# Optimization experiments

Hardware: AMD Instinct MI355X
Metric: run time of the kernel (lower is better)

Reference implementation:

```python
import jax, jax.numpy as jnp
import numpy as np

NUM_EXPERTS = 8
HIDDEN = 1024
INTER = 2048
RANK = 8
LORA_ALPHA = 16
SCALING = LORA_ALPHA / RANK  # 2.0


def setup_inputs() -> dict:
    key = jax.random.key(0)
    ks = jax.random.split(key, 7)
    return {
        "hidden_states": jax.random.normal(ks[0], (NUM_EXPERTS * 1024, HIDDEN), jnp.float32),
        "gate_up_proj": jax.random.normal(ks[1], (NUM_EXPERTS, HIDDEN, 2 * INTER), jnp.float32) * 0.02,
        "down_proj": jax.random.normal(ks[2], (NUM_EXPERTS, INTER, HIDDEN), jnp.float32) * 0.02,
        "lora_A_gu": jax.random.normal(ks[3], (RANK, HIDDEN), jnp.float32) * 0.02,
        "lora_B_gu": jax.random.normal(ks[4], (2 * INTER, RANK), jnp.float32) * 0.02,
        "lora_A_dn": jax.random.normal(ks[5], (RANK, INTER), jnp.float32) * 0.02,
        "lora_B_dn": jax.random.normal(ks[6], (1024, RANK), jnp.float32) * 0.02,
    }


def reference(hidden_states, gate_up_proj, down_proj, lora_A_gu, lora_B_gu, lora_A_dn, lora_B_dn):
    E, H, F2 = gate_up_proj.shape
    x = hidden_states.reshape(E, -1, H)  # [E, T, H]
    # per-expert GEMM + shared LoRA adapter (dropout inactive at eval)
    gate_up = jnp.einsum('eth,ehf->etf', x, gate_up_proj)
    gate_up = gate_up + ((x @ lora_A_gu.T) @ lora_B_gu.T) * SCALING  # [E, T, 2I]
    gate, up = jnp.split(gate_up, 2, axis=-1)
    hidden = up * jax.nn.silu(gate)  # SwiGLU, [E, T, I]
    out = jnp.einsum('eti,eih->eth', hidden, down_proj)
    out = out + ((hidden @ lora_A_dn.T) @ lora_B_dn.T) * SCALING
    return out.reshape(-1, H)
```

## Files before the change

kernel.cpp:

```cpp
#include <hip/hip_runtime.h>
#include <math.h>


#define NE 8
#define TT 1024
#define HH 1024
#define II 2048
#define FF2 4096
#define RR 8
#define NROW (NE * TT)
#define SCAL 2.0f

typedef __bf16 bf16x8 __attribute__((ext_vector_type(8)));
typedef float f32x4 __attribute__((ext_vector_type(4)));

#define GLOAD16(g, l)                                                        \
  __builtin_amdgcn_global_load_lds((const __attribute__((address_space(1))) void*)(g), \
                                   (__attribute__((address_space(3))) void*)(l), 16, 0, 0)
#define BARRIER __builtin_amdgcn_s_barrier()
#define SB0 __builtin_amdgcn_sched_barrier(0)
#define WAITV2 asm volatile("s_waitcnt vmcnt(2)" ::: "memory")
#define WAITV0 asm volatile("s_waitcnt vmcnt(0)" ::: "memory")
#define WAITL0 asm volatile("s_waitcnt lgkmcnt(0)" ::: "memory")

__device__ __forceinline__ unsigned short f2bf(float f) {
  unsigned int u = __float_as_uint(f);
  u += 0x7fffu + ((u >> 16) & 1u);
  return (unsigned short)(u >> 16);
}
__device__ __forceinline__ float dot4(float4 a, float4 b) {
  return a.x * b.x + a.y * b.y + a.z * b.z + a.w * b.w;
}

__global__ __launch_bounds__(256) void convx_kernel(const float* __restrict__ x,
                                                    unsigned short* __restrict__ xb) {
  const int i = blockIdx.x * 256 + threadIdx.x;
  const float4 a = *(const float4*)(x + (size_t)i * 8);
  const float4 b = *(const float4*)(x + (size_t)i * 8 + 4);
  union { unsigned short u[8]; uint4 v; } pk;
  pk.u[0] = f2bf(a.x); pk.u[1] = f2bf(a.y); pk.u[2] = f2bf(a.z); pk.u[3] = f2bf(a.w);
  pk.u[4] = f2bf(b.x); pk.u[5] = f2bf(b.y); pk.u[6] = f2bf(b.z); pk.u[7] = f2bf(b.w);
  *(uint4*)(xb + (size_t)i * 8) = pk.v;
}

__global__ __launch_bounds__(256) void transconv_gu_kernel(const float* __restrict__ W,
                                                           unsigned short* __restrict__ WT) {
  __shared__ float ts[64][65];
  const int bid = blockIdx.x;
  const int nt = bid & 63, kt = (bid >> 6) & 15, e = bid >> 10;
  const float* Win = W + (size_t)e * HH * FF2 + (size_t)(kt * 64) * FF2 + nt * 64;
  const int tid = threadIdx.x;
#pragma unroll
  for (int l = 0; l < 4; ++l) {
    const int idx = tid + l * 256, r = idx >> 4, c4 = idx & 15;
    const float4 v = *(const float4*)(Win + (size_t)r * FF2 + c4 * 4);
    ts[r][c4 * 4 + 0] = v.x; ts[r][c4 * 4 + 1] = v.y;
    ts[r][c4 * 4 + 2] = v.z; ts[r][c4 * 4 + 3] = v.w;
  }
  __syncthreads();
  unsigned short* We = WT + (size_t)e * FF2 * HH;
#pragma unroll
  for (int l = 0; l < 2; ++l) {
    const int idx = tid + l * 256, j = idx >> 3, q = idx & 7;
    int orow;
    if (nt < 32) orow = (nt * 4 + (j >> 4)) * 32 + (j & 15);
    else         orow = ((nt - 32) * 4 + (j >> 4)) * 32 + 16 + (j & 15);
    union { unsigned short u[8]; uint4 v; } pk;
#pragma unroll
    for (int kk = 0; kk < 8; ++kk) pk.u[kk] = f2bf(ts[q * 8 + kk][j]);
    *(uint4*)(We + (size_t)orow * HH + kt * 64 + q * 8) = pk.v;
  }
}

__global__ __launch_bounds__(256) void transconv_dn_kernel(const float* __restrict__ W,
                                                           unsigned short* __restrict__ WT) {
  __shared__ float ts[64][65];
  const int bid = blockIdx.x;
  const int nt = bid & 15, kt = (bid >> 4) & 31, e = bid >> 9;
  const float* Win = W + (size_t)e * II * HH + (size_t)(kt * 64) * HH + nt * 64;
  const int tid = threadIdx.x;
#pragma unroll
  for (int l = 0; l < 4; ++l) {
    const int idx = tid + l * 256, r = idx >> 4, c4 = idx & 15;
    const float4 v = *(const float4*)(Win + (size_t)r * HH + c4 * 4);
    ts[r][c4 * 4 + 0] = v.x; ts[r][c4 * 4 + 1] = v.y;
    ts[r][c4 * 4 + 2] = v.z; ts[r][c4 * 4 + 3] = v.w;
  }
  __syncthreads();
  unsigned short* Wout = WT + (size_t)e * HH * II + (size_t)(nt * 64) * II + kt * 64;
#pragma unroll
  for (int l = 0; l < 2; ++l) {
    const int idx = tid + l * 256, j = idx >> 3, q = idx & 7;
    union { unsigned short u[8]; uint4 v; } pk;
#pragma unroll
    for (int kk = 0; kk < 8; ++kk) pk.u[kk] = f2bf(ts[q * 8 + kk][j]);
    *(uint4*)(Wout + (size_t)j * II + q * 8) = pk.v;
  }
}

template <int K>
__global__ __launch_bounds__(256) void rowdot_kernel(const float* __restrict__ x,
                                                     const float* __restrict__ A,
                                                     float* __restrict__ xa) {
  const int w = threadIdx.x >> 6, lane = threadIdx.x & 63;
  const int t = blockIdx.x * 4 + w;
  const float* xrow = x + (size_t)t * K;
  float acc[RR];
#pragma unroll
  for (int r = 0; r < RR; ++r) acc[r] = 0.f;
#pragma unroll
  for (int c = 0; c < K / 256; ++c) {
    const float4 xv = *(const float4*)(xrow + c * 256 + lane * 4);
#pragma unroll
    for (int r = 0; r < RR; ++r) {
      const float4 av = *(const float4*)(A + (size_t)r * K + c * 256 + lane * 4);
      acc[r] += dot4(xv, av);
    }
  }
#pragma unroll
  for (int r = 0; r < RR; ++r) {
    float v = acc[r];
#pragma unroll
    for (int off = 32; off > 0; off >>= 1) v += __shfl_down(v, off, 64);
    if (lane == 0) xa[(size_t)t * RR + r] = v;
  }
}

__global__ __launch_bounds__(256) void rowdot_bf16_kernel(const unsigned short* __restrict__ h,
                                                          const float* __restrict__ A,
                                                          float* __restrict__ ha) {
  const int w = threadIdx.x >> 6, lane = threadIdx.x & 63;
  const int t = blockIdx.x * 4 + w;
  const unsigned short* hrow = h + (size_t)t * II;
  float acc[RR];
#pragma unroll
  for (int r = 0; r < RR; ++r) acc[r] = 0.f;
#pragma unroll
  for (int c = 0; c < II / 512; ++c) {
    const uint4 v = *(const uint4*)(hrow + c * 512 + lane * 8);
    float xv[8];
    xv[0] = __uint_as_float(v.x << 16); xv[1] = __uint_as_float(v.x & 0xffff0000u);
    xv[2] = __uint_as_float(v.y << 16); xv[3] = __uint_as_float(v.y & 0xffff0000u);
    xv[4] = __uint_as_float(v.z << 16); xv[5] = __uint_as_float(v.z & 0xffff0000u);
    xv[6] = __uint_as_float(v.w << 16); xv[7] = __uint_as_float(v.w & 0xffff0000u);
#pragma unroll
    for (int r = 0; r < RR; ++r) {
      const float4 a0 = *(const float4*)(A + (size_t)r * II + c * 512 + lane * 8);
      const float4 a1 = *(const float4*)(A + (size_t)r * II + c * 512 + lane * 8 + 4);
      acc[r] += xv[0] * a0.x + xv[1] * a0.y + xv[2] * a0.z + xv[3] * a0.w +
                xv[4] * a1.x + xv[5] * a1.y + xv[6] * a1.z + xv[7] * a1.w;
    }
  }
#pragma unroll
  for (int r = 0; r < RR; ++r) {
    float v = acc[r];
#pragma unroll
    for (int off = 32; off > 0; off >>= 1) v += __shfl_down(v, off, 64);
    if (lane == 0) ha[(size_t)t * RR + r] = v;
  }
}

__global__ __launch_bounds__(256) void gemm1_8p_kernel(
    const unsigned short* __restrict__ xb, const unsigned short* __restrict__ WguT,
    const float* __restrict__ xa, const float* __restrict__ Bgu,
    unsigned short* __restrict__ hidden) {
  __shared__ unsigned short sm[2][16384];

  const int bid = blockIdx.x;
  const int e = bid & 7;
  const int s = bid >> 3;
  const int g = s >> 6, wq = s & 63;
  const int tt = wq >> 3, it = (g << 3) | (wq & 7);
  const int t0 = e * TT + tt * 128;
  const unsigned short* Ag = xb + (size_t)t0 * HH;
  const unsigned short* Bg = WguT + (size_t)e * FF2 * HH + (size_t)(it * 128) * HH;

  const int tid = threadIdx.x;
  const int w = tid >> 6, lane = tid & 63;
  const int wr = w >> 1, wc = w & 1;
  const int lrow = lane & 15, lkg = lane >> 4;

  auto stageA = [&](int buf, int kt, int h) {
#pragma unroll
    for (int l = 0; l < 2; ++l) {
      const int i = tid + l * 256;
      const int r = i >> 3, sl = i & 7;
      const int row = h * 64 + r;
      GLOAD16((const char*)(Ag + (size_t)row * HH + kt * 64 + ((sl ^ (row & 7)) << 3)),
              (char*)&sm[buf][0] + row * 128 + sl * 16);
    }
  };
  auto stageB = [&](int buf, int kt, int h) {
#pragma unroll
    for (int l = 0; l < 2; ++l) {
      const int i = tid + l * 256;
      const int r = i >> 3, sl = i & 7;
      const int row = h * 64 + r;
      GLOAD16((const char*)(Bg + (size_t)row * HH + kt * 64 + ((sl ^ (row & 7)) << 3)),
              (char*)&sm[buf][0] + 16384 + row * 128 + sl * 16);
    }
  };
  auto ldA = [&](int p, int mIdx, int s2) -> bf16x8 {
    const int row = wr * 64 + mIdx * 16 + lrow;
    const int sl = (s2 * 4 + lkg) ^ (row & 7);
    return *(const bf16x8*)((const char*)&sm[p][0] + row * 128 + sl * 16);
  };
  auto ldB = [&](int p, int nj, int s2) -> bf16x8 {
    const int row = wc * 64 + nj * 16 + lrow;
    const int sl = (s2 * 4 + lkg) ^ (row & 7);
    return *(const bf16x8*)((const char*)&sm[p][0] + 16384 + row * 128 + sl * 16);
  };

  f32x4 acc[4][4];
#pragma unroll
  for (int i = 0; i < 4; ++i)
#pragma unroll
    for (int j = 0; j < 4; ++j) acc[i][j] = (f32x4)(0.f);

  stageA(0, 0, 0); stageA(0, 0, 1); stageB(0, 0, 0); stageB(0, 0, 1);

  bf16x8 af[2][2], bfr[2][2];
  const int NT = HH / 64;
  for (int t = 0; t < NT; ++t) {
    const int p = t & 1, q = p ^ 1;
    const bool pf = (t + 1 < NT);
    if (pf) { stageA(q, t + 1, 0); WAITV2; } else { WAITV0; }
    SB0; BARRIER;
#pragma unroll
    for (int mi = 0; mi < 2; ++mi) { af[mi][0] = ldA(p, mi, 0); af[mi][1] = ldA(p, mi, 1); }
#pragma unroll
    for (int nj = 0; nj < 2; ++nj) { bfr[nj][0] = ldB(p, nj, 0); bfr[nj][1] = ldB(p, nj, 1); }
    BARRIER; WAITL0; SB0;
    __builtin_amdgcn_s_setprio(1);
#pragma unroll
    for (int mi = 0; mi < 2; ++mi)
#pragma unroll
      for (int nj = 0; nj < 2; ++nj)
#pragma unroll
        for (int s2 = 0; s2 < 2; ++s2)
          acc[mi][nj] = __builtin_amdgcn_mfma_f32_16x16x32_bf16(af[mi][s2], bfr[nj][s2], acc[mi][nj], 0, 0, 0);
    __builtin_amdgcn_s_setprio(0); SB0; BARRIER;
    if (pf) stageA(q, t + 1, 1);
#pragma unroll
    for (int nj = 0; nj < 2; ++nj) { bfr[nj][0] = ldB(p, 2 + nj, 0); bfr[nj][1] = ldB(p, 2 + nj, 1); }
    BARRIER; WAITL0; SB0;
    __builtin_amdgcn_s_setprio(1);
#pragma unroll
    for (int mi = 0; mi < 2; ++mi)
#pragma unroll
      for (int nj = 0; nj < 2; ++nj)
#pragma unroll
        for (int s2 = 0; s2 < 2; ++s2)
          acc[mi][2 + nj] = __builtin_amdgcn_mfma_f32_16x16x32_bf16(af[mi][s2], bfr[nj][s2], acc[mi][2 + nj], 0, 0, 0);
    __builtin_amdgcn_s_setprio(0); SB0; BARRIER;
    if (pf) stageB(q, t + 1, 0);
#pragma unroll
    for (int mi = 0; mi < 2; ++mi) { af[mi][0] = ldA(p, 2 + mi, 0); af[mi][1] = ldA(p, 2 + mi, 1); }
    BARRIER; WAITL0; SB0;
    __builtin_amdgcn_s_setprio(1);
#pragma unroll
    for (int mi = 0; mi < 2; ++mi)
#pragma unroll
      for (int nj = 0; nj < 2; ++nj)
#pragma unroll
        for (int s2 = 0; s2 < 2; ++s2)
          acc[2 + mi][2 + nj] = __builtin_amdgcn_mfma_f32_16x16x32_bf16(af[mi][s2], bfr[nj][s2], acc[2 + mi][2 + nj], 0, 0, 0);
    __builtin_amdgcn_s_setprio(0); SB0; BARRIER;
    if (pf) stageB(q, t + 1, 1);
#pragma unroll
    for (int nj = 0; nj < 2; ++nj) { bfr[nj][0] = ldB(p, nj, 0); bfr[nj][1] = ldB(p, nj, 1); }
    BARRIER; WAITL0; SB0;
    __builtin_amdgcn_s_setprio(1);
#pragma unroll
    for (int mi = 0; mi < 2; ++mi)
#pragma unroll
      for (int nj = 0; nj < 2; ++nj)
#pragma unroll
        for (int s2 = 0; s2 < 2; ++s2)
          acc[2 + mi][nj] = __builtin_amdgcn_mfma_f32_16x16x32_bf16(af[mi][s2], bfr[nj][s2], acc[2 + mi][nj], 0, 0, 0);
    __builtin_amdgcn_s_setprio(0); SB0; BARRIER;
  }

  const float4* xa4 = (const float4*)xa;
  const float4* B4 = (const float4*)Bgu;
#pragma unroll
  for (int f = 0; f < 2; ++f) {
    const int gc = it * 64 + (wc * 2 + f) * 16 + lrow;
    const float4 bg0 = B4[gc * 2], bg1 = B4[gc * 2 + 1];
    const float4 bu0 = B4[(II + gc) * 2], bu1 = B4[(II + gc) * 2 + 1];
#pragma unroll
    for (int m = 0; m < 4; ++m) {
      const int tb = t0 + wr * 64 + m * 16 + lkg * 4;
#pragma unroll
      for (int j = 0; j < 4; ++j) {
        const int trow = tb + j;
        const float4 xr0 = xa4[trow * 2], xr1 = xa4[trow * 2 + 1];
        const float gv = acc[m][f * 2 + 0][j] + SCAL * (dot4(xr0, bg0) + dot4(xr1, bg1));
        const float uv = acc[m][f * 2 + 1][j] + SCAL * (dot4(xr0, bu0) + dot4(xr1, bu1));
        const float sg = gv / (1.f + __expf(-gv));
        hidden[(size_t)trow * II + gc] = f2bf(uv * sg);
      }
    }
  }
}

__global__ __launch_bounds__(256) void gemm2_8p_kernel(
    const unsigned short* __restrict__ hid, const unsigned short* __restrict__ WdnT,
    const float* __restrict__ ha, const float* __restrict__ Bdn,
    float* __restrict__ out) {
  __shared__ unsigned short sm[2][16384];

  const int bid = blockIdx.x;
  const int e = bid & 7;
  const int s = bid >> 3;
  const int g = s >> 4, wq = s & 15;
  const int tt = (g >> 1) * 4 + (wq >> 2);
  const int ht = (g & 1) * 4 + (wq & 3);
  const int t0 = e * TT + tt * 128;
  const int h0 = ht * 128;
  const unsigned short* Ag = hid + (size_t)t0 * II;
  const unsigned short* Bg = WdnT + (size_t)e * HH * II + (size_t)h0 * II;

  const int tid = threadIdx.x;
  const int w = tid >> 6, lane = tid & 63;
  const int wr = w >> 1, wc = w & 1;
  const int lrow = lane & 15, lkg = lane >> 4;

  auto stageA = [&](int buf, int kt, int h) {
#pragma unroll
    for (int l = 0; l < 2; ++l) {
      const int i = tid + l * 256;
      const int r = i >> 3, sl = i & 7;
      const int row = h * 64 + r;
      GLOAD16((const char*)(Ag + (size_t)row * II + kt * 64 + ((sl ^ (row & 7)) << 3)),
              (char*)&sm[buf][0] + row * 128 + sl * 16);
    }
  };
  auto stageB = [&](int buf, int kt, int h) {
#pragma unroll
    for (int l = 0; l < 2; ++l) {
      const int i = tid + l * 256;
      const int r = i >> 3, sl = i & 7;
      const int row = h * 64 + r;
      GLOAD16((const char*)(Bg + (size_t)row * II + kt * 64 + ((sl ^ (row & 7)) << 3)),
              (char*)&sm[buf][0] + 16384 + row * 128 + sl * 16);
    }
  };
  auto ldA = [&](int p, int mIdx, int s2) -> bf16x8 {
    const int row = wr * 64 + mIdx * 16 + lrow;
    const int sl = (s2 * 4 + lkg) ^ (row & 7);
    return *(const bf16x8*)((const char*)&sm[p][0] + row * 128 + sl * 16);
  };
  auto ldB = [&](int p, int nj, int s2) -> bf16x8 {
    const int row = wc * 64 + nj * 16 + lrow;
    const int sl = (s2 * 4 + lkg) ^ (row & 7);
    return *(const bf16x8*)((const char*)&sm[p][0] + 16384 + row * 128 + sl * 16);
  };

  f32x4 acc[4][4];
#pragma unroll
  for (int i = 0; i < 4; ++i)
#pragma unroll
    for (int j = 0; j < 4; ++j) acc[i][j] = (f32x4)(0.f);

  stageA(0, 0, 0); stageA(0, 0, 1); stageB(0, 0, 0); stageB(0, 0, 1);

  bf16x8 af[2][2], bfr[2][2];
  const int NT = II / 64;
  for (int t = 0; t < NT; ++t) {
    const int p = t & 1, q = p ^ 1;
    const bool pf = (t + 1 < NT);
    if (pf) { stageA(q, t + 1, 0); WAITV2; } else { WAITV0; }
    SB0; BARRIER;
#pragma unroll
    for (int mi = 0; mi < 2; ++mi) { af[mi][0] = ldA(p, mi, 0); af[mi][1] = ldA(p, mi, 1); }
#pragma unroll
    for (int nj = 0; nj < 2; ++nj) { bfr[nj][0] = ldB(p, nj, 0); bfr[nj][1] = ldB(p, nj, 1); }
    BARRIER; WAITL0; SB0;
    __builtin_amdgcn_s_setprio(1);
#pragma unroll
    for (int mi = 0; mi < 2; ++mi)
#pragma unroll
      for (int nj = 0; nj < 2; ++nj)
#pragma unroll
        for (int s2 = 0; s2 < 2; ++s2)
          acc[mi][nj] = __builtin_amdgcn_mfma_f32_16x16x32_bf16(af[mi][s2], bfr[nj][s2], acc[mi][nj], 0, 0, 0);
    __builtin_amdgcn_s_setprio(0); SB0; BARRIER;
    if (pf) stageA(q, t + 1, 1);
#pragma unroll
    for (int nj = 0; nj < 2; ++nj) { bfr[nj][0] = ldB(p, 2 + nj, 0); bfr[nj][1] = ldB(p, 2 + nj, 1); }
    BARRIER; WAITL0; SB0;
    __builtin_amdgcn_s_setprio(1);
#pragma unroll
    for (int mi = 0; mi < 2; ++mi)
#pragma unroll
      for (int nj = 0; nj < 2; ++nj)
#pragma unroll
        for (int s2 = 0; s2 < 2; ++s2)
          acc[mi][2 + nj] = __builtin_amdgcn_mfma_f32_16x16x32_bf16(af[mi][s2], bfr[nj][s2], acc[mi][2 + nj], 0, 0, 0);
    __builtin_amdgcn_s_setprio(0); SB0; BARRIER;
    if (pf) stageB(q, t + 1, 0);
#pragma unroll
    for (int mi = 0; mi < 2; ++mi) { af[mi][0] = ldA(p, 2 + mi, 0); af[mi][1] = ldA(p, 2 + mi, 1); }
    BARRIER; WAITL0; SB0;
    __builtin_amdgcn_s_setprio(1);
#pragma unroll
    for (int mi = 0; mi < 2; ++mi)
#pragma unroll
      for (int nj = 0; nj < 2; ++nj)
#pragma unroll
        for (int s2 = 0; s2 < 2; ++s2)
          acc[2 + mi][2 + nj] = __builtin_amdgcn_mfma_f32_16x16x32_bf16(af[mi][s2], bfr[nj][s2], acc[2 + mi][2 + nj], 0, 0, 0);
    __builtin_amdgcn_s_setprio(0); SB0; BARRIER;
    if (pf) stageB(q, t + 1, 1);
#pragma unroll
    for (int nj = 0; nj < 2; ++nj) { bfr[nj][0] = ldB(p, nj, 0); bfr[nj][1] = ldB(p, nj, 1); }
    BARRIER; WAITL0; SB0;
    __builtin_amdgcn_s_setprio(1);
#pragma unroll
    for (int mi = 0; mi < 2; ++mi)
#pragma unroll
      for (int nj = 0; nj < 2; ++nj)
#pragma unroll
        for (int s2 = 0; s2 < 2; ++s2)
          acc[2 + mi][nj] = __builtin_amdgcn_mfma_f32_16x16x32_bf16(af[mi][s2], bfr[nj][s2], acc[2 + mi][nj], 0, 0, 0);
    __builtin_amdgcn_s_setprio(0); SB0; BARRIER;
  }

  const float4* ha4 = (const float4*)ha;
  const float4* B4 = (const float4*)Bdn;
#pragma unroll
  for (int nj = 0; nj < 4; ++nj) {
    const int col = h0 + wc * 64 + nj * 16 + lrow;
    const float4 b0 = B4[col * 2], b1 = B4[col * 2 + 1];
#pragma unroll
    for (int m = 0; m < 4; ++m) {
      const int tb = t0 + wr * 64 + m * 16 + lkg * 4;
#pragma unroll
      for (int j = 0; j < 4; ++j) {
        const int trow = tb + j;
        const float4 hr0 = ha4[trow * 2], hr1 = ha4[trow * 2 + 1];
        out[(size_t)trow * HH + col] = acc[m][nj][j] + SCAL * (dot4(hr0, b0) + dot4(hr1, b1));
      }
    }
  }
}

__global__ __launch_bounds__(256) void gemm1_conv_kernel(const float* __restrict__ x,
                                                         const float* __restrict__ Wgu,
                                                         const float* __restrict__ xa,
                                                         const float* __restrict__ Bgu,
                                                         unsigned short* __restrict__ hidden) {
  __shared__ unsigned short As[128][40];
  __shared__ unsigned short Bs[128][40];
  const int bid = blockIdx.x;
  const int e = bid >> 8, rem = bid & 255, tt = rem >> 5, it = rem & 31;
  const int t0 = e * TT + tt * 128, i0 = it * 64;
  const float* Wg = Wgu + (size_t)e * HH * FF2;
  const int tid = threadIdx.x, w = tid >> 6, lane = tid & 63;
  const int wr = w >> 1, wc = w & 1, lrow = lane & 15, lk = (lane >> 4) * 8;
  f32x4 acc[4][4];
#pragma unroll
  for (int i = 0; i < 4; ++i)
#pragma unroll
    for (int j = 0; j < 4; ++j) acc[i][j] = (f32x4)(0.f);
  for (int k0 = 0; k0 < HH; k0 += 32) {
#pragma unroll
    for (int l = 0; l < 4; ++l) {
      const int idx = tid + l * 256, row = idx >> 3, kq = idx & 7;
      const float4 v = *(const float4*)(x + (size_t)(t0 + row) * HH + k0 + kq * 4);
      ushort4 p; p.x = f2bf(v.x); p.y = f2bf(v.y); p.z = f2bf(v.z); p.w = f2bf(v.w);
      *(ushort4*)&As[row][kq * 4] = p;
    }
#pragma unroll
    for (int l = 0; l < 2; ++l) {
      const int idx = tid + l * 256, col = idx & 127, kq8 = idx >> 7;
      const int gcol = i0 + (col & 63) + ((col >> 6) * II);
      union { unsigned short u[8]; uint4 v; } pk;
#pragma unroll
      for (int kk = 0; kk < 8; ++kk) pk.u[kk] = f2bf(Wg[(size_t)(k0 + kq8 * 8 + kk) * FF2 + gcol]);
      *(uint4*)&Bs[col][kq8 * 8] = pk.v;
    }
    __syncthreads();
    bf16x8 af[4], bfr[4];
#pragma unroll
    for (int mi = 0; mi < 4; ++mi) af[mi] = *(const bf16x8*)&As[wr * 64 + mi * 16 + lrow][lk];
#pragma unroll
    for (int nj = 0; nj < 4; ++nj) {
      const int c = (nj < 2) ? (wc * 32 + nj * 16) : (64 + wc * 32 + (nj - 2) * 16);
      bfr[nj] = *(const bf16x8*)&Bs[c + lrow][lk];
    }
#pragma unroll
    for (int mi = 0; mi < 4; ++mi)
#pragma unroll
      for (int nj = 0; nj < 4; ++nj)
        acc[mi][nj] = __builtin_amdgcn_mfma_f32_16x16x32_bf16(af[mi], bfr[nj], acc[mi][nj], 0, 0, 0);
    __syncthreads();
  }
  const float4* xa4 = (const float4*)xa;
  const float4* B4 = (const float4*)Bgu;
#pragma unroll
  for (int nj = 0; nj < 2; ++nj) {
    const int coln = i0 + wc * 32 + nj * 16 + lrow;
    const float4 bg0 = B4[coln * 2], bg1 = B4[coln * 2 + 1];
    const float4 bu0 = B4[(II + coln) * 2], bu1 = B4[(II + coln) * 2 + 1];
#pragma unroll
    for (int mi = 0; mi < 4; ++mi) {
      const int tb = t0 + wr * 64 + mi * 16 + (lane >> 4) * 4;
#pragma unroll
      for (int j = 0; j < 4; ++j) {
        const int t = tb + j;
        const float4 xr0 = xa4[t * 2], xr1 = xa4[t * 2 + 1];
        const float g = acc[mi][nj][j] + SCAL * (dot4(xr0, bg0) + dot4(xr1, bg1));
        const float u = acc[mi][nj + 2][j] + SCAL * (dot4(xr0, bu0) + dot4(xr1, bu1));
        const float s = g / (1.f + __expf(-g));
        hidden[(size_t)t * II + coln] = f2bf(u * s);
      }
    }
  }
}

__global__ __launch_bounds__(256) void gemm2_conv_kernel(const unsigned short* __restrict__ hid,
                                                         const float* __restrict__ Wdn,
                                                         const float* __restrict__ ha,
                                                         const float* __restrict__ Bdn,
                                                         float* __restrict__ out) {
  __shared__ unsigned short As[128][40];
  __shared__ unsigned short Bs[128][40];
  const int bid = blockIdx.x;
  const int e = bid >> 6, rem = bid & 63, tt = rem >> 3, ht = rem & 7;
  const int t0 = e * TT + tt * 128, h0 = ht * 128;
  const float* Wd = Wdn + (size_t)e * II * HH;
  const int tid = threadIdx.x, w = tid >> 6, lane = tid & 63;
  const int wr = w >> 1, wc = w & 1, lrow = lane & 15, lk = (lane >> 4) * 8;
  f32x4 acc[4][4];
#pragma unroll
  for (int i = 0; i < 4; ++i)
#pragma unroll
    for (int j = 0; j < 4; ++j) acc[i][j] = (f32x4)(0.f);
  for (int k0 = 0; k0 < II; k0 += 32) {
#pragma unroll
    for (int l = 0; l < 2; ++l) {
      const int idx = tid + l * 256, row = idx >> 2, kq8 = idx & 3;
      *(uint4*)&As[row][kq8 * 8] = *(const uint4*)(hid + (size_t)(t0 + row) * II + k0 + kq8 * 8);
    }
#pragma unroll
    for (int l = 0; l < 2; ++l) {
      const int idx = tid + l * 256, col = idx & 127, kq8 = idx >> 7;
      union { unsigned short u[8]; uint4 v; } pk;
#pragma unroll
      for (int kk = 0; kk < 8; ++kk) pk.u[kk] = f2bf(Wd[(size_t)(k0 + kq8 * 8 + kk) * HH + h0 + col]);
      *(uint4*)&Bs[col][kq8 * 8] = pk.v;
    }
    __syncthreads();
    bf16x8 af[4], bfr[4];
#pragma unroll
    for (int mi = 0; mi < 4; ++mi) af[mi] = *(const bf16x8*)&As[wr * 64 + mi * 16 + lrow][lk];
#pragma unroll
    for (int nj = 0; nj < 4; ++nj) bfr[nj] = *(const bf16x8*)&Bs[wc * 64 + nj * 16 + lrow][lk];
#pragma unroll
    for (int mi = 0; mi < 4; ++mi)
#pragma unroll
      for (int nj = 0; nj < 4; ++nj)
        acc[mi][nj] = __builtin_amdgcn_mfma_f32_16x16x32_bf16(af[mi], bfr[nj], acc[mi][nj], 0, 0, 0);
    __syncthreads();
  }
  const float4* ha4 = (const float4*)ha;
  const float4* B4 = (const float4*)Bdn;
#pragma unroll
  for (int nj = 0; nj < 4; ++nj) {
    const int coln = h0 + wc * 64 + nj * 16 + lrow;
    const float4 b0 = B4[coln * 2], b1 = B4[coln * 2 + 1];
#pragma unroll
    for (int mi = 0; mi < 4; ++mi) {
      const int tb = t0 + wr * 64 + mi * 16 + (lane >> 4) * 4;
#pragma unroll
      for (int j = 0; j < 4; ++j) {
        const int t = tb + j;
        const float4 hr0 = ha4[t * 2], hr1 = ha4[t * 2 + 1];
        out[(size_t)t * HH + coln] = acc[mi][nj][j] + SCAL * (dot4(hr0, b0) + dot4(hr1, b1));
      }
    }
  }
}

extern "C" void kernel_launch(void* const* d_in, const int* in_sizes, int n_in,
                              void* d_out, int out_size, void* d_ws, size_t ws_size,
                              hipStream_t stream) {
  const float* x   = (const float*)d_in[0];
  const float* Wgu = (const float*)d_in[1];
  const float* Wdn = (const float*)d_in[2];
  const float* Agu = (const float*)d_in[3];
  const float* Bgu = (const float*)d_in[4];
  const float* Adn = (const float*)d_in[5];
  const float* Bdn = (const float*)d_in[6];
  float* out = (float*)d_out;

  char* ws = (char*)d_ws;
  unsigned short* hidden = (unsigned short*)ws;
  const size_t OFF_XB  = (size_t)NROW * II * 2;
  const size_t OFF_WGU = OFF_XB + (size_t)NROW * HH * 2;
  const size_t OFF_WDN = OFF_WGU + (size_t)NE * FF2 * HH * 2;
  const size_t OFF_XA  = OFF_WDN + (size_t)NE * HH * II * 2;
  const size_t OFF_HA  = OFF_XA + (size_t)NROW * RR * 4;
  const size_t NEED    = OFF_HA + (size_t)NROW * RR * 4;

  if (ws_size >= NEED) {
    unsigned short* xb   = (unsigned short*)(ws + OFF_XB);
    unsigned short* WguT = (unsigned short*)(ws + OFF_WGU);
    unsigned short* WdnT = (unsigned short*)(ws + OFF_WDN);
    float* xa = (float*)(ws + OFF_XA);
    float* ha = (float*)(ws + OFF_HA);

    convx_kernel<<<(NROW * HH) / (256 * 8), 256, 0, stream>>>(x, xb);
    transconv_gu_kernel<<<NE * 16 * 64, 256, 0, stream>>>(Wgu, WguT);
    transconv_dn_kernel<<<NE * 32 * 16, 256, 0, stream>>>(Wdn, WdnT);
    rowdot_kernel<HH><<<NROW / 4, 256, 0, stream>>>(x, Agu, xa);
    gemm1_8p_kernel<<<NE * 8 * 32, 256, 0, stream>>>(xb, WguT, xa, Bgu, hidden);
    rowdot_bf16_kernel<<<NROW / 4, 256, 0, stream>>>(hidden, Adn, ha);
    gemm2_8p_kernel<<<NE * 8 * 8, 256, 0, stream>>>(hidden, WdnT, ha, Bdn, out);
  } else {
    float* xa = (float*)(ws + OFF_XB);
    float* ha = xa + (size_t)NROW * RR;
    rowdot_kernel<HH><<<NROW / 4, 256, 0, stream>>>(x, Agu, xa);
    gemm1_conv_kernel<<<NE * 8 * 32, 256, 0, stream>>>(x, Wgu, xa, Bgu, hidden);
    rowdot_bf16_kernel<<<NROW / 4, 256, 0, stream>>>(hidden, Adn, ha);
    gemm2_conv_kernel<<<NE * 8 * 8, 256, 0, stream>>>(hidden, Wdn, ha, Bdn, out);
  }
}
```

Before: 395.6 us.

## Collapse four-phase interleaved GEMM main loop into single prefetch-then-compute stage

```diff
diff --git a/kernel.cpp b/kernel.cpp
--- a/kernel.cpp
+++ b/kernel.cpp
@@ -19,7 +19,7 @@
                                    (__attribute__((address_space(3))) void*)(l), 16, 0, 0)
 #define BARRIER __builtin_amdgcn_s_barrier()
 #define SB0 __builtin_amdgcn_sched_barrier(0)
-#define WAITV2 asm volatile("s_waitcnt vmcnt(2)" ::: "memory")
+#define WAITV8 asm volatile("s_waitcnt vmcnt(8)" ::: "memory")
 #define WAITV0 asm volatile("s_waitcnt vmcnt(0)" ::: "memory")
 #define WAITL0 asm volatile("s_waitcnt lgkmcnt(0)" ::: "memory")
 
@@ -219,65 +219,31 @@
 
   stageA(0, 0, 0); stageA(0, 0, 1); stageB(0, 0, 0); stageB(0, 0, 1);
 
-  bf16x8 af[2][2], bfr[2][2];
   const int NT = HH / 64;
   for (int t = 0; t < NT; ++t) {
     const int p = t & 1, q = p ^ 1;
-    const bool pf = (t + 1 < NT);
-    if (pf) { stageA(q, t + 1, 0); WAITV2; } else { WAITV0; }
+    if (t + 1 < NT) {
+      stageA(q, t + 1, 0); stageA(q, t + 1, 1);
+      stageB(q, t + 1, 0); stageB(q, t + 1, 1);
+      WAITV8;
+    } else {
+      WAITV0;
+    }
     SB0; BARRIER;
-#pragma unroll
-    for (int mi = 0; mi < 2; ++mi) { af[mi][0] = ldA(p, mi, 0); af[mi][1] = ldA(p, mi, 1); }
-#pragma unroll
-    for (int nj = 0; nj < 2; ++nj) { bfr[nj][0] = ldB(p, nj, 0); bfr[nj][1] = ldB(p, nj, 1); }
-    BARRIER; WAITL0; SB0;
+    bf16x8 af[4][2], bfr[4][2];
+#pragma unroll
+    for (int mi = 0; mi < 4; ++mi) { af[mi][0] = ldA(p, mi, 0); af[mi][1] = ldA(p, mi, 1); }
+#pragma unroll
+    for (int nj = 0; nj < 4; ++nj) { bfr[nj][0] = ldB(p, nj, 0); bfr[nj][1] = ldB(p, nj, 1); }
+    WAITL0; SB0;
     __builtin_amdgcn_s_setprio(1);
 #pragma unroll
-    for (int mi = 0; mi < 2; ++mi)
-#pragma unroll
-      for (int nj = 0; nj < 2; ++nj)
+    for (int mi = 0; mi < 4; ++mi)
+#pragma unroll
+      for (int nj = 0; nj < 4; ++nj)
 #pragma unroll
         for (int s2 = 0; s2 < 2; ++s2)
           acc[mi][nj] = __builtin_amdgcn_mfma_f32_16x16x32_bf16(af[mi][s2], bfr[nj][s2], acc[mi][nj], 0, 0, 0);
-    __builtin_amdgcn_s_setprio(0); SB0; BARRIER;
-    if (pf) stageA(q, t + 1, 1);
-#pragma unroll
-    for (int nj = 0; nj < 2; ++nj) { bfr[nj][0] = ldB(p, 2 + nj, 0); bfr[nj][1] = ldB(p, 2 + nj, 1); }
-    BARRIER; WAITL0; SB0;
-    __builtin_amdgcn_s_setprio(1);
-#pragma unroll
-    for (int mi = 0; mi < 2; ++mi)
-#pragma unroll
-      for (int nj = 0; nj < 2; ++nj)
-#pragma unroll
-        for (int s2 = 0; s2 < 2; ++s2)
-          acc[mi][2 + nj] = __builtin_amdgcn_mfma_f32_16x16x32_bf16(af[mi][s2], bfr[nj][s2], acc[mi][2 + nj], 0, 0, 0);
-    __builtin_amdgcn_s_setprio(0); SB0; BARRIER;
-    if (pf) stageB(q, t + 1, 0);
-#pragma unroll
-    for (int mi = 0; mi < 2; ++mi) { af[mi][0] = ldA(p, 2 + mi, 0); af[mi][1] = ldA(p, 2 + mi, 1); }
-    BARRIER; WAITL0; SB0;
-    __builtin_amdgcn_s_setprio(1);
-#pragma unroll
-    for (int mi = 0; mi < 2; ++mi)
-#pragma unroll
-      for (int nj = 0; nj < 2; ++nj)
-#pragma unroll
-        for (int s2 = 0; s2 < 2; ++s2)
-          acc[2 + mi][2 + nj] = __builtin_amdgcn_mfma_f32_16x16x32_bf16(af[mi][s2], bfr[nj][s2], acc[2 + mi][2 + nj], 0, 0, 0);
-    __builtin_amdgcn_s_setprio(0); SB0; BARRIER;
-    if (pf) stageB(q, t + 1, 1);
-#pragma unroll
-    for (int nj = 0; nj < 2; ++nj) { bfr[nj][0] = ldB(p, nj, 0); bfr[nj][1] = ldB(p, nj, 1); }
-    BARRIER; WAITL0; SB0;
-    __builtin_amdgcn_s_setprio(1);
-#pragma unroll
-    for (int mi = 0; mi < 2; ++mi)
-#pragma unroll
-      for (int nj = 0; nj < 2; ++nj)
-#pragma unroll
-        for (int s2 = 0; s2 < 2; ++s2)
-          acc[2 + mi][nj] = __builtin_amdgcn_mfma_f32_16x16x32_bf16(af[mi][s2], bfr[nj][s2], acc[2 + mi][nj], 0, 0, 0);
     __builtin_amdgcn_s_setprio(0); SB0; BARRIER;
   }
 
@@ -365,65 +331,31 @@
 
   stageA(0, 0, 0); stageA(0, 0, 1); stageB(0, 0, 0); stageB(0, 0, 1);
 
-  bf16x8 af[2][2], bfr[2][2];
   const int NT = II / 64;
   for (int t = 0; t < NT; ++t) {
     const int p = t & 1, q = p ^ 1;
-    const bool pf = (t + 1 < NT);
-    if (pf) { stageA(q, t + 1, 0); WAITV2; } else { WAITV0; }
+    if (t + 1 < NT) {
+      stageA(q, t + 1, 0); stageA(q, t + 1, 1);
+      stageB(q, t + 1, 0); stageB(q, t + 1, 1);
+      WAITV8;
+    } else {
+      WAITV0;
+    }
     SB0; BARRIER;
-#pragma unroll
-    for (int mi = 0; mi < 2; ++mi) { af[mi][0] = ldA(p, mi, 0); af[mi][1] = ldA(p, mi, 1); }
-#pragma unroll
-    for (int nj = 0; nj < 2; ++nj) { bfr[nj][0] = ldB(p, nj, 0); bfr[nj][1] = ldB(p, nj, 1); }
-    BARRIER; WAITL0; SB0;
+    bf16x8 af[4][2], bfr[4][2];
+#pragma unroll
+    for (int mi = 0; mi < 4; ++mi) { af[mi][0] = ldA(p, mi, 0); af[mi][1] = ldA(p, mi, 1); }
+#pragma unroll
+    for (int nj = 0; nj < 4; ++nj) { bfr[nj][0] = ldB(p, nj, 0); bfr[nj][1] = ldB(p, nj, 1); }
+    WAITL0; SB0;
     __builtin_amdgcn_s_setprio(1);
 #pragma unroll
-    for (int mi = 0; mi < 2; ++mi)
-#pragma unroll
-      for (int nj = 0; nj < 2; ++nj)
+    for (int mi = 0; mi < 4; ++mi)
+#pragma unroll
+      for (int nj = 0; nj < 4; ++nj)
 #pragma unroll
         for (int s2 = 0; s2 < 2; ++s2)
           acc[mi][nj] = __builtin_amdgcn_mfma_f32_16x16x32_bf16(af[mi][s2], bfr[nj][s2], acc[mi][nj], 0, 0, 0);
-    __builtin_amdgcn_s_setprio(0); SB0; BARRIER;
-    if (pf) stageA(q, t + 1, 1);
-#pragma unroll
-    for (int nj = 0; nj < 2; ++nj) { bfr[nj][0] = ldB(p, 2 + nj, 0); bfr[nj][1] = ldB(p, 2 + nj, 1); }
-    BARRIER; WAITL0; SB0;
-    __builtin_amdgcn_s_setprio(1);
-#pragma unroll
-    for (int mi = 0; mi < 2; ++mi)
-#pragma unroll
-      for (int nj = 0; nj < 2; ++nj)
-#pragma unroll
-        for (int s2 = 0; s2 < 2; ++s2)
-          acc[mi][2 + nj] = __builtin_amdgcn_mfma_f32_16x16x32_bf16(af[mi][s2], bfr[nj][s2], acc[mi][2 + nj], 0, 0, 0);
-    __builtin_amdgcn_s_setprio(0); SB0; BARRIER;
-    if (pf) stageB(q, t + 1, 0);
-#pragma unroll
-    for (int mi = 0; mi < 2; ++mi) { af[mi][0] = ldA(p, 2 + mi, 0); af[mi][1] = ldA(p, 2 + mi, 1); }
-    BARRIER; WAITL0; SB0;
-    __builtin_amdgcn_s_setprio(1);
-#pragma unroll
-    for (int mi = 0; mi < 2; ++mi)
-#pragma unroll
-      for (int nj = 0; nj < 2; ++nj)
-#pragma unroll
-        for (int s2 = 0; s2 < 2; ++s2)
-          acc[2 + mi][2 + nj] = __builtin_amdgcn_mfma_f32_16x16x32_bf16(af[mi][s2], bfr[nj][s2], acc[2 + mi][2 + nj], 0, 0, 0);
-    __builtin_amdgcn_s_setprio(0); SB0; BARRIER;
-    if (pf) stageB(q, t + 1, 1);
-#pragma unroll
-    for (int nj = 0; nj < 2; ++nj) { bfr[nj][0] = ldB(p, nj, 0); bfr[nj][1] = ldB(p, nj, 1); }
-    BARRIER; WAITL0; SB0;
-    __builtin_amdgcn_s_setprio(1);
-#pragma unroll
-    for (int mi = 0; mi < 2; ++mi)
-#pragma unroll
-      for (int nj = 0; nj < 2; ++nj)
-#pragma unroll
-        for (int s2 = 0; s2 < 2; ++s2)
-          acc[2 + mi][nj] = __builtin_amdgcn_mfma_f32_16x16x32_bf16(af[mi][s2], bfr[nj][s2], acc[2 + mi][nj], 0, 0, 0);
     __builtin_amdgcn_s_setprio(0); SB0; BARRIER;
   }
 
```

New measurement: 357.6 us (median of 2 runs). -9.6%, faster.
